# Performance work log

Hardware: AMD Instinct MI355X
Metric: run time of the kernel (lower is better)

## Reference

```python
import jax, jax.numpy as jnp
import numpy as np

B, S, W = 4, 4096, 41
SDR_N = 2048
HIDDEN = 2048
EPS = 1e-5


def setup_inputs() -> dict:
    key = jax.random.key(0)
    k1, k2 = jax.random.split(key)
    input_ids = jax.random.randint(k1, (B, S, W), 0, SDR_N, dtype=jnp.int64)
    proj_w = jax.random.normal(k2, (HIDDEN, SDR_N), dtype=jnp.float32) * 0.02
    gamma = jnp.ones((HIDDEN,), dtype=jnp.float32)
    beta = jnp.zeros((HIDDEN,), dtype=jnp.float32)
    return {"input_ids": input_ids, "proj_w": proj_w, "gamma": gamma, "beta": beta}


def reference(input_ids, proj_w, gamma, beta):
    b, s, w = input_ids.shape
    # scatter_ with src=1 SETS (not adds) -> duplicates collapse to 1
    bi = jnp.arange(b)[:, None, None]
    si = jnp.arange(s)[None, :, None]
    x_sparse = jnp.zeros((b, s, SDR_N), dtype=proj_w.dtype).at[bi, si, input_ids].set(1.0)
    # dense projection: [B,S,N] @ [N,H]
    x = jnp.einsum('bsn,hn->bsh', x_sparse, proj_w)
    # LayerNorm over last dim
    mu = jnp.mean(x, axis=-1, keepdims=True)
    var = jnp.var(x, axis=-1, keepdims=True)
    x = (x - mu) * jax.lax.rsqrt(var + EPS)
    return x * gamma + beta
```

## Files before the change

### kernel.cpp

```cpp
#include <hip/hip_runtime.h>
#include <hip/hip_bf16.h>

#define BB      4
#define SS      4096
#define WW      41
#define SDRN    2048
#define HID     2048
#define NTOK    (BB * SS)
#define EPS_LN  1e-5f
#define NSLICE  4
#define SLICE_H 512

typedef float f32x4 __attribute__((ext_vector_type(4)));


__global__ __launch_bounds__(256) void transpose_cvt(const float* __restrict__ in,
                                                     __hip_bfloat16* __restrict__ out) {
    __shared__ float tile[32][33];
    int x = blockIdx.x * 32 + threadIdx.x;
    int y = blockIdx.y * 32 + threadIdx.y;
#pragma unroll
    for (int j = 0; j < 32; j += 8)
        tile[threadIdx.y + j][threadIdx.x] = in[(size_t)(y + j) * SDRN + x];
    __syncthreads();
    x = blockIdx.y * 32 + threadIdx.x;
    y = blockIdx.x * 32 + threadIdx.y;
#pragma unroll
    for (int j = 0; j < 32; j += 8)
        out[(size_t)(y + j) * HID + x] = __float2bfloat16(tile[threadIdx.x][threadIdx.y + j]);
}

__global__ __launch_bounds__(256) void sdr_gather_p1(
    const int* __restrict__ ids, const __hip_bfloat16* __restrict__ Wt,
    float* __restrict__ x, float2* __restrict__ partials) {
    const int b     = blockIdx.x;
    const int sub   = b & 1;
    const int slice = (b & 7) >> 1;
    const int tg    = ((b >> 3) << 1) | sub;
    const int wave  = threadIdx.x >> 6;
    const int lane  = threadIdx.x & 63;
    const int token = tg * 4 + wave;

    int myid = 0;
    if (lane < WW) myid = ids[(size_t)token * WW + lane];
    int keep = (lane < WW) ? 1 : 0;
#pragma unroll
    for (int j = 0; j < WW; ++j) {
        const int idj = __shfl(myid, j);
        if (j < lane && lane < WW && idj == myid) keep = 0;
    }

    float acc[8] = {0.f, 0.f, 0.f, 0.f, 0.f, 0.f, 0.f, 0.f};
    const unsigned int* base =
        (const unsigned int*)Wt + (size_t)slice * (SLICE_H / 2) + (size_t)lane * 4;

    for (int i = 0; i < WW; ++i) {
        const int idi = __shfl(myid, i);
        const int ki  = __shfl(keep, i);
        if (!ki) continue;
        const uint4 u = *(const uint4*)(base + (size_t)idi * (HID / 2));
        acc[0] += __uint_as_float(u.x << 16);
        acc[1] += __uint_as_float(u.x & 0xffff0000u);
        acc[2] += __uint_as_float(u.y << 16);
        acc[3] += __uint_as_float(u.y & 0xffff0000u);
        acc[4] += __uint_as_float(u.z << 16);
        acc[5] += __uint_as_float(u.z & 0xffff0000u);
        acc[6] += __uint_as_float(u.w << 16);
        acc[7] += __uint_as_float(u.w & 0xffff0000u);
    }

    float s = 0.f, s2 = 0.f;
#pragma unroll
    for (int j = 0; j < 8; ++j) { s += acc[j]; s2 += acc[j] * acc[j]; }
#pragma unroll
    for (int off = 1; off < 64; off <<= 1) {
        s  += __shfl_xor(s, off);
        s2 += __shfl_xor(s2, off);
    }
    if (lane == 0) {
        float2 p; p.x = s; p.y = s2;
        partials[(size_t)token * NSLICE + slice] = p;
    }

    float* xr = x + (size_t)token * HID + slice * SLICE_H + lane * 8;
    f32x4 v0; v0.x = acc[0]; v0.y = acc[1]; v0.z = acc[2]; v0.w = acc[3];
    f32x4 v1; v1.x = acc[4]; v1.y = acc[5]; v1.z = acc[6]; v1.w = acc[7];
    __builtin_nontemporal_store(v0, (f32x4*)xr);
    __builtin_nontemporal_store(v1, (f32x4*)xr + 1);
}

__global__ __launch_bounds__(256) void sdr_ln_p2(
    float* __restrict__ x, const float2* __restrict__ partials,
    const float* __restrict__ gamma, const float* __restrict__ beta) {
    const int token = blockIdx.x;
    const int tid   = threadIdx.x;

    float s = 0.f, s2 = 0.f;
#pragma unroll
    for (int j = 0; j < NSLICE; ++j) {
        const float2 p = partials[(size_t)token * NSLICE + j];
        s += p.x; s2 += p.y;
    }
    const float mean = s * (1.0f / HID);
    const float var  = s2 * (1.0f / HID) - mean * mean;
    const float rstd = rsqrtf(var + EPS_LN);

    float4*       xr = (float4*)(x + (size_t)token * HID) + tid * 2;
    const float4* g4 = (const float4*)gamma + tid * 2;
    const float4* b4 = (const float4*)beta  + tid * 2;
    float4 a = xr[0], b = xr[1];
    const float4 g0 = g4[0], g1 = g4[1];
    const float4 be0 = b4[0], be1 = b4[1];
    a.x = (a.x - mean) * rstd * g0.x + be0.x;
    a.y = (a.y - mean) * rstd * g0.y + be0.y;
    a.z = (a.z - mean) * rstd * g0.z + be0.z;
    a.w = (a.w - mean) * rstd * g0.w + be0.w;
    b.x = (b.x - mean) * rstd * g1.x + be1.x;
    b.y = (b.y - mean) * rstd * g1.y + be1.y;
    b.z = (b.z - mean) * rstd * g1.z + be1.z;
    b.w = (b.w - mean) * rstd * g1.w + be1.w;
    xr[0] = a;
    xr[1] = b;
}

__global__ __launch_bounds__(256) void sdr_gather_ln_notr(
    const int* __restrict__ ids, const float* __restrict__ W,
    const float* __restrict__ gamma, const float* __restrict__ beta,
    float* __restrict__ out) {
    const int token = blockIdx.x;
    const int tid   = threadIdx.x;

    __shared__ int   s_ids[WW];
    __shared__ int   s_keep[WW];
    __shared__ float s_red[8];

    if (tid < WW) s_ids[tid] = ids[(size_t)token * WW + tid];
    __syncthreads();
    if (tid < WW) {
        const int v = s_ids[tid];
        int keep = 1;
        for (int j = 0; j < tid; ++j)
            if (s_ids[j] == v) { keep = 0; break; }
        s_keep[tid] = keep;
    }
    __syncthreads();

    float acc[8] = {0.f};
    for (int i = 0; i < WW; ++i) {
        if (!s_keep[i]) continue;
        const int id = s_ids[i];
#pragma unroll
        for (int j = 0; j < 8; ++j) {
            const int h = tid * 8 + j;
            acc[j] += W[(size_t)h * SDRN + id];
        }
    }
    float s = 0.f, s2 = 0.f;
#pragma unroll
    for (int j = 0; j < 8; ++j) { s += acc[j]; s2 += acc[j] * acc[j]; }
#pragma unroll
    for (int off = 1; off < 64; off <<= 1) {
        s  += __shfl_xor(s, off);
        s2 += __shfl_xor(s2, off);
    }
    const int wave = tid >> 6;
    if ((tid & 63) == 0) { s_red[wave] = s; s_red[4 + wave] = s2; }
    __syncthreads();
    const float ts   = s_red[0] + s_red[1] + s_red[2] + s_red[3];
    const float ts2  = s_red[4] + s_red[5] + s_red[6] + s_red[7];
    const float mean = ts * (1.0f / HID);
    const float var  = ts2 * (1.0f / HID) - mean * mean;
    const float rstd = rsqrtf(var + EPS_LN);

#pragma unroll
    for (int j = 0; j < 8; ++j) {
        const int h = tid * 8 + j;
        out[(size_t)token * HID + h] = (acc[j] - mean) * rstd * gamma[h] + beta[h];
    }
}

extern "C" void kernel_launch(void* const* d_in, const int* in_sizes, int n_in,
                              void* d_out, int out_size, void* d_ws, size_t ws_size,
                              hipStream_t stream) {
    const int*   ids    = (const int*)d_in[0];
    const float* proj_w = (const float*)d_in[1];
    const float* gamma  = (const float*)d_in[2];
    const float* beta   = (const float*)d_in[3];
    float*       out    = (float*)d_out;

    const size_t wt_bytes   = (size_t)SDRN * HID * sizeof(__hip_bfloat16);
    const size_t part_bytes = (size_t)NTOK * NSLICE * sizeof(float2);

    if (ws_size >= wt_bytes + part_bytes) {
        __hip_bfloat16* Wt = (__hip_bfloat16*)d_ws;
        float2* partials   = (float2*)((char*)d_ws + wt_bytes);

        dim3 tb(32, 8), tg(SDRN / 32, HID / 32);
        transpose_cvt<<<tg, tb, 0, stream>>>(proj_w, Wt);
        sdr_gather_p1<<<NTOK, 256, 0, stream>>>(ids, Wt, out, partials);
        sdr_ln_p2<<<NTOK, 256, 0, stream>>>(out, partials, gamma, beta);
    } else {
        sdr_gather_ln_notr<<<NTOK, 256, 0, stream>>>(ids, proj_w, gamma, beta, out);
    }
}
```

Measured before the change: 199.1 us.

## Compact unique ids, batch gathers four at a time, store bf16 intermediate

The gather kernel compacts the deduplicated ids into shared memory via ballot and popcount, pads the list to a multiple of four with a zero row, and issues four independent row loads per iteration using readlane indices. This raises memory-level parallelism and removes the per-iteration skip branches. When workspace allows, the pre-norm activations are written as bf16 to a scratch buffer instead of fp32 in the output. The second pass then reads half the bytes and writes the output. The bf16 intermediate adds rounding error before normalization, and the code needs extra workspace plus one more tiny launch.

```diff
diff --git a/kernel.cpp b/kernel.cpp
--- a/kernel.cpp
+++ b/kernel.cpp
@@ -10,9 +10,16 @@
 #define EPS_LN  1e-5f
 #define NSLICE  4
 #define SLICE_H 512
-
-typedef float f32x4 __attribute__((ext_vector_type(4)));
-
+#define PADID   SDRN
+#define TROWS   (SDRN + 1)
+
+typedef float        f32x2 __attribute__((ext_vector_type(2)));
+typedef float        f32x4 __attribute__((ext_vector_type(4)));
+typedef unsigned int u32x4 __attribute__((ext_vector_type(4)));
+
+static __device__ __forceinline__ unsigned short bf16bits(float f) {
+    return __builtin_bit_cast(unsigned short, __float2bfloat16(f));
+}
 
 __global__ __launch_bounds__(256) void transpose_cvt(const float* __restrict__ in,
                                                      __hip_bfloat16* __restrict__ out) {
@@ -30,9 +37,15 @@
         out[(size_t)(y + j) * HID + x] = __float2bfloat16(tile[threadIdx.x][threadIdx.y + j]);
 }
 
+__global__ void zero_pad_row(__hip_bfloat16* __restrict__ Wt) {
+    u32x4 z = {0u, 0u, 0u, 0u};
+    *((u32x4*)(Wt + (size_t)PADID * HID) + threadIdx.x) = z;
+}
+
+template <bool XBF>
 __global__ __launch_bounds__(256) void sdr_gather_p1(
     const int* __restrict__ ids, const __hip_bfloat16* __restrict__ Wt,
-    float* __restrict__ x, float2* __restrict__ partials) {
+    void* __restrict__ xout, float2* __restrict__ partials) {
     const int b     = blockIdx.x;
     const int sub   = b & 1;
     const int slice = (b & 7) >> 1;
@@ -41,37 +54,51 @@
     const int lane  = threadIdx.x & 63;
     const int token = tg * 4 + wave;
 
-    int myid = 0;
-    if (lane < WW) myid = ids[(size_t)token * WW + lane];
+    __shared__ int s_uids[4][44];
+
+    int myid = (lane < WW) ? ids[(size_t)token * WW + lane] : 0;
     int keep = (lane < WW) ? 1 : 0;
 #pragma unroll
     for (int j = 0; j < WW; ++j) {
         const int idj = __shfl(myid, j);
         if (j < lane && lane < WW && idj == myid) keep = 0;
     }
-
-    float acc[8] = {0.f, 0.f, 0.f, 0.f, 0.f, 0.f, 0.f, 0.f};
-    const unsigned int* base =
-        (const unsigned int*)Wt + (size_t)slice * (SLICE_H / 2) + (size_t)lane * 4;
-
-    for (int i = 0; i < WW; ++i) {
-        const int idi = __shfl(myid, i);
-        const int ki  = __shfl(keep, i);
-        if (!ki) continue;
-        const uint4 u = *(const uint4*)(base + (size_t)idi * (HID / 2));
-        acc[0] += __uint_as_float(u.x << 16);
-        acc[1] += __uint_as_float(u.x & 0xffff0000u);
-        acc[2] += __uint_as_float(u.y << 16);
-        acc[3] += __uint_as_float(u.y & 0xffff0000u);
-        acc[4] += __uint_as_float(u.z << 16);
-        acc[5] += __uint_as_float(u.z & 0xffff0000u);
-        acc[6] += __uint_as_float(u.w << 16);
-        acc[7] += __uint_as_float(u.w & 0xffff0000u);
-    }
-
-    float s = 0.f, s2 = 0.f;
-#pragma unroll
-    for (int j = 0; j < 8; ++j) { s += acc[j]; s2 += acc[j] * acc[j]; }
+    const unsigned long long km = __ballot(keep);
+    const int nkeep = __popcll(km);
+    const int nk4   = (nkeep + 3) & ~3;
+    if (keep) {
+        const int rank = __popcll(km & ((1ull << lane) - 1ull));
+        s_uids[wave][rank] = myid;
+    }
+    if (lane >= nkeep && lane < nk4) s_uids[wave][lane] = PADID;
+    const int cid = s_uids[wave][lane < 44 ? lane : 0];
+
+    f32x2 a0 = {0.f, 0.f}, a1 = {0.f, 0.f}, a2 = {0.f, 0.f}, a3 = {0.f, 0.f};
+    const int lofs = slice * SLICE_H + lane * 8;
+
+#define ACC8(u)                                                                 \
+    { f32x2 t;                                                                  \
+      t.x = __uint_as_float((u).x << 16); t.y = __uint_as_float((u).x & 0xffff0000u); a0 += t; \
+      t.x = __uint_as_float((u).y << 16); t.y = __uint_as_float((u).y & 0xffff0000u); a1 += t; \
+      t.x = __uint_as_float((u).z << 16); t.y = __uint_as_float((u).z & 0xffff0000u); a2 += t; \
+      t.x = __uint_as_float((u).w << 16); t.y = __uint_as_float((u).w & 0xffff0000u); a3 += t; }
+
+    for (int i = 0; i < nk4; i += 4) {
+        const int id0 = __builtin_amdgcn_readlane(cid, i);
+        const int id1 = __builtin_amdgcn_readlane(cid, i + 1);
+        const int id2 = __builtin_amdgcn_readlane(cid, i + 2);
+        const int id3 = __builtin_amdgcn_readlane(cid, i + 3);
+        const u32x4 u0 = *(const u32x4*)((const unsigned int*)(Wt + (size_t)id0 * HID + lofs));
+        const u32x4 u1 = *(const u32x4*)((const unsigned int*)(Wt + (size_t)id1 * HID + lofs));
+        const u32x4 u2 = *(const u32x4*)((const unsigned int*)(Wt + (size_t)id2 * HID + lofs));
+        const u32x4 u3 = *(const u32x4*)((const unsigned int*)(Wt + (size_t)id3 * HID + lofs));
+        ACC8(u0); ACC8(u1); ACC8(u2); ACC8(u3);
+    }
+#undef ACC8
+
+    float s  = a0.x + a0.y + a1.x + a1.y + a2.x + a2.y + a3.x + a3.y;
+    float s2 = a0.x * a0.x + a0.y * a0.y + a1.x * a1.x + a1.y * a1.y +
+               a2.x * a2.x + a2.y * a2.y + a3.x * a3.x + a3.y * a3.y;
 #pragma unroll
     for (int off = 1; off < 64; off <<= 1) {
         s  += __shfl_xor(s, off);
@@ -82,14 +109,67 @@
         partials[(size_t)token * NSLICE + slice] = p;
     }
 
-    float* xr = x + (size_t)token * HID + slice * SLICE_H + lane * 8;
-    f32x4 v0; v0.x = acc[0]; v0.y = acc[1]; v0.z = acc[2]; v0.w = acc[3];
-    f32x4 v1; v1.x = acc[4]; v1.y = acc[5]; v1.z = acc[6]; v1.w = acc[7];
-    __builtin_nontemporal_store(v0, (f32x4*)xr);
-    __builtin_nontemporal_store(v1, (f32x4*)xr + 1);
-}
-
-__global__ __launch_bounds__(256) void sdr_ln_p2(
+    if (XBF) {
+        u32x4 o;
+        o.x = (unsigned)bf16bits(a0.x) | ((unsigned)bf16bits(a0.y) << 16);
+        o.y = (unsigned)bf16bits(a1.x) | ((unsigned)bf16bits(a1.y) << 16);
+        o.z = (unsigned)bf16bits(a2.x) | ((unsigned)bf16bits(a2.y) << 16);
+        o.w = (unsigned)bf16bits(a3.x) | ((unsigned)bf16bits(a3.y) << 16);
+        __hip_bfloat16* xb = (__hip_bfloat16*)xout;
+        __builtin_nontemporal_store(o, (u32x4*)(xb + (size_t)token * HID + lofs));
+    } else {
+        float* xf = (float*)xout;
+        f32x4 v0; v0.x = a0.x; v0.y = a0.y; v0.z = a1.x; v0.w = a1.y;
+        f32x4 v1; v1.x = a2.x; v1.y = a2.y; v1.z = a3.x; v1.w = a3.y;
+        f32x4* xr = (f32x4*)(xf + (size_t)token * HID + lofs);
+        __builtin_nontemporal_store(v0, xr);
+        __builtin_nontemporal_store(v1, xr + 1);
+    }
+}
+
+__global__ __launch_bounds__(256) void sdr_ln_p2_bf(
+    const __hip_bfloat16* __restrict__ xbf, const float2* __restrict__ partials,
+    const float* __restrict__ gamma, const float* __restrict__ beta,
+    float* __restrict__ out) {
+    const int token = blockIdx.x;
+    const int tid   = threadIdx.x;
+
+    float s = 0.f, s2 = 0.f;
+#pragma unroll
+    for (int j = 0; j < NSLICE; ++j) {
+        const float2 p = partials[(size_t)token * NSLICE + j];
+        s += p.x; s2 += p.y;
+    }
+    const float mean = s * (1.0f / HID);
+    const float var  = s2 * (1.0f / HID) - mean * mean;
+    const float rstd = rsqrtf(var + EPS_LN);
+
+    const u32x4 u = *((const u32x4*)(xbf + (size_t)token * HID) + tid);
+    float xv[8];
+    xv[0] = __uint_as_float(u.x << 16); xv[1] = __uint_as_float(u.x & 0xffff0000u);
+    xv[2] = __uint_as_float(u.y << 16); xv[3] = __uint_as_float(u.y & 0xffff0000u);
+    xv[4] = __uint_as_float(u.z << 16); xv[5] = __uint_as_float(u.z & 0xffff0000u);
+    xv[6] = __uint_as_float(u.w << 16); xv[7] = __uint_as_float(u.w & 0xffff0000u);
+
+    const f32x4* g4 = (const f32x4*)gamma + tid * 2;
+    const f32x4* b4 = (const f32x4*)beta  + tid * 2;
+    const f32x4 g0 = g4[0], g1 = g4[1];
+    const f32x4 be0 = b4[0], be1 = b4[1];
+    f32x4 r0, r1;
+    r0.x = (xv[0] - mean) * rstd * g0.x + be0.x;
+    r0.y = (xv[1] - mean) * rstd * g0.y + be0.y;
+    r0.z = (xv[2] - mean) * rstd * g0.z + be0.z;
+    r0.w = (xv[3] - mean) * rstd * g0.w + be0.w;
+    r1.x = (xv[4] - mean) * rstd * g1.x + be1.x;
+    r1.y = (xv[5] - mean) * rstd * g1.y + be1.y;
+    r1.z = (xv[6] - mean) * rstd * g1.z + be1.z;
+    r1.w = (xv[7] - mean) * rstd * g1.w + be1.w;
+    f32x4* o4 = (f32x4*)(out + (size_t)token * HID) + tid * 2;
+    __builtin_nontemporal_store(r0, o4);
+    __builtin_nontemporal_store(r1, o4 + 1);
+}
+
+__global__ __launch_bounds__(256) void sdr_ln_p2_inplace(
     float* __restrict__ x, const float2* __restrict__ partials,
     const float* __restrict__ gamma, const float* __restrict__ beta) {
     const int token = blockIdx.x;
@@ -108,19 +188,19 @@
     float4*       xr = (float4*)(x + (size_t)token * HID) + tid * 2;
     const float4* g4 = (const float4*)gamma + tid * 2;
     const float4* b4 = (const float4*)beta  + tid * 2;
-    float4 a = xr[0], b = xr[1];
+    float4 a = xr[0], bq = xr[1];
     const float4 g0 = g4[0], g1 = g4[1];
     const float4 be0 = b4[0], be1 = b4[1];
-    a.x = (a.x - mean) * rstd * g0.x + be0.x;
-    a.y = (a.y - mean) * rstd * g0.y + be0.y;
-    a.z = (a.z - mean) * rstd * g0.z + be0.z;
-    a.w = (a.w - mean) * rstd * g0.w + be0.w;
-    b.x = (b.x - mean) * rstd * g1.x + be1.x;
-    b.y = (b.y - mean) * rstd * g1.y + be1.y;
-    b.z = (b.z - mean) * rstd * g1.z + be1.z;
-    b.w = (b.w - mean) * rstd * g1.w + be1.w;
+    a.x  = (a.x  - mean) * rstd * g0.x + be0.x;
+    a.y  = (a.y  - mean) * rstd * g0.y + be0.y;
+    a.z  = (a.z  - mean) * rstd * g0.z + be0.z;
+    a.w  = (a.w  - mean) * rstd * g0.w + be0.w;
+    bq.x = (bq.x - mean) * rstd * g1.x + be1.x;
+    bq.y = (bq.y - mean) * rstd * g1.y + be1.y;
+    bq.z = (bq.z - mean) * rstd * g1.z + be1.z;
+    bq.w = (bq.w - mean) * rstd * g1.w + be1.w;
     xr[0] = a;
-    xr[1] = b;
+    xr[1] = bq;
 }
 
 __global__ __launch_bounds__(256) void sdr_gather_ln_notr(
@@ -188,17 +268,28 @@
     const float* beta   = (const float*)d_in[3];
     float*       out    = (float*)d_out;
 
-    const size_t wt_bytes   = (size_t)SDRN * HID * sizeof(__hip_bfloat16);
+    const size_t wt_bytes   = (size_t)TROWS * HID * sizeof(__hip_bfloat16);
     const size_t part_bytes = (size_t)NTOK * NSLICE * sizeof(float2);
-
-    if (ws_size >= wt_bytes + part_bytes) {
+    const size_t xbf_bytes  = (size_t)NTOK * HID * sizeof(__hip_bfloat16);
+    const size_t need_core  = wt_bytes + part_bytes;
+    const size_t need_full  = need_core + xbf_bytes;
+
+    if (ws_size >= need_core) {
         __hip_bfloat16* Wt = (__hip_bfloat16*)d_ws;
         float2* partials   = (float2*)((char*)d_ws + wt_bytes);
 
         dim3 tb(32, 8), tg(SDRN / 32, HID / 32);
         transpose_cvt<<<tg, tb, 0, stream>>>(proj_w, Wt);
-        sdr_gather_p1<<<NTOK, 256, 0, stream>>>(ids, Wt, out, partials);
-        sdr_ln_p2<<<NTOK, 256, 0, stream>>>(out, partials, gamma, beta);
+        zero_pad_row<<<1, 256, 0, stream>>>(Wt);
+
+        if (ws_size >= need_full) {
+            __hip_bfloat16* xbf = (__hip_bfloat16*)((char*)d_ws + need_core);
+            sdr_gather_p1<true><<<NTOK, 256, 0, stream>>>(ids, Wt, xbf, partials);
+            sdr_ln_p2_bf<<<NTOK, 256, 0, stream>>>(xbf, partials, gamma, beta, out);
+        } else {
+            sdr_gather_p1<false><<<NTOK, 256, 0, stream>>>(ids, Wt, out, partials);
+            sdr_ln_p2_inplace<<<NTOK, 256, 0, stream>>>(out, partials, gamma, beta);
+        }
     } else {
         sdr_gather_ln_notr<<<NTOK, 256, 0, stream>>>(ids, proj_w, gamma, beta, out);
     }
```

Result: faster. 167.0 us (-16.2%).
